# Kernel optimization log

Hardware: AMD Instinct MI355X
Metric: run time of the kernel (lower is better)

The kernel has to match this reference:

```python
import jax, jax.numpy as jnp
import numpy as np

D_MODEL = 1024
N_HEADS = 16
BLOCK = 256
NEG = -1e9


def setup_inputs() -> dict:
    key = jax.random.key(0)
    ks = jax.random.split(key, 5)
    B, S, D = 4, 4096, D_MODEL
    scale = 0.02
    inp = {
        "x": jax.random.normal(ks[0], (B, S, D), dtype=jnp.float32),
        "Wq": jax.random.normal(ks[1], (D, D), dtype=jnp.float32) * scale,
        "bq": jnp.zeros((D,), dtype=jnp.float32),
        "Wk": jax.random.normal(ks[2], (D, D), dtype=jnp.float32) * scale,
        "bk": jnp.zeros((D,), dtype=jnp.float32),
        "Wv": jax.random.normal(ks[3], (D, D), dtype=jnp.float32) * scale,
        "bv": jnp.zeros((D,), dtype=jnp.float32),
        "Wo": jax.random.normal(ks[4], (D, D), dtype=jnp.float32) * scale,
        "bo": jnp.zeros((D,), dtype=jnp.float32),
    }
    return inp


def _local_attention(x, Wq, bq, Wk, bk, Wv, bv, Wo, bo):
    B, S, D = x.shape
    h, dh, bs = N_HEADS, D // N_HEADS, BLOCK
    pad_len = (bs - S % bs) % bs
    if pad_len > 0:
        x = jnp.pad(x, ((0, 0), (0, pad_len), (0, 0)))
    Sp = x.shape[1]
    nb = Sp // bs
    # independent local blocks: [B*nb, bs, D]
    xb = x.reshape(B * nb, bs, D)

    def proj(W, b):
        # [N, bs, D] -> [N, h, bs, dh]
        y = xb @ W + b
        return y.reshape(B * nb, bs, h, dh).transpose(0, 2, 1, 3)

    q = proj(Wq, bq)
    k = proj(Wk, bk)
    v = proj(Wv, bv)

    scores = jnp.einsum('nhqd,nhkd->nhqk', q, k) / jnp.sqrt(jnp.asarray(dh, x.dtype))
    causal = jnp.tril(jnp.ones((bs, bs), dtype=bool))  # block-local causal mask
    scores = jnp.where(causal, scores, jnp.asarray(NEG, x.dtype))
    probs = jax.nn.softmax(scores, axis=-1)
    out = jnp.einsum('nhqk,nhkd->nhqd', probs, v)
    out = out.transpose(0, 2, 1, 3).reshape(B, Sp, D)
    if pad_len > 0:
        out = out[:, :S, :]
    return out @ Wo + bo


def reference(x, Wq, bq, Wk, bk, Wv, bv, Wo, bo):
    return _local_attention(x, Wq, bq, Wk, bk, Wv, bv, Wo, bo)
```

## Files before the change

kernel.cpp:

```cpp
#include <hip/hip_runtime.h>
#include <cstdint>
#include <cstddef>

typedef unsigned short u16;
typedef __attribute__((ext_vector_type(8))) short s16x8;
typedef __attribute__((ext_vector_type(8))) unsigned short u16x8;
typedef __attribute__((ext_vector_type(4))) float f32x4;

#define D_MODEL 1024
#define DH 64
#define BS 256

__device__ __forceinline__ u16 f2bf(float f) {
  union { float f; unsigned int i; } x; x.f = f;
  unsigned int r = x.i + 0x7fffu + ((x.i >> 16) & 1u);
  return (u16)(r >> 16);
}

__device__ __forceinline__ void gl_lds16(const u16* g, u16* l) {
  __builtin_amdgcn_global_load_lds((const __attribute__((address_space(1))) void*)g,
                                   (__attribute__((address_space(3))) void*)l, 16, 0, 0);
}

__device__ __forceinline__ unsigned lds_off(const u16* p) {
  return (unsigned)(uintptr_t)(const __attribute__((address_space(3))) u16*)p;
}

__global__ __launch_bounds__(256) void cast_x(const float* __restrict__ x, u16* __restrict__ xb) {
  int i = (blockIdx.x * 256 + threadIdx.x) * 8;
  f32x4 a0 = *(const f32x4*)(x + i);
  f32x4 a1 = *(const f32x4*)(x + i + 4);
  u16x8 v;
#pragma unroll
  for (int j = 0; j < 4; ++j) { v[j] = f2bf(a0[j]); v[j + 4] = f2bf(a1[j]); }
  *(u16x8*)(xb + i) = v;
}

__global__ __launch_bounds__(256) void transpose_w(const float* __restrict__ w0,
                                                   const float* __restrict__ w1,
                                                   const float* __restrict__ w2,
                                                   const float* __restrict__ w3,
                                                   u16* __restrict__ out) {
  __shared__ u16 tile[64][65];
  const int z = blockIdx.z;
  const float* W = (z == 0) ? w0 : (z == 1) ? w1 : (z == 2) ? w2 : w3;
  u16* O = out + (size_t)z * (D_MODEL * D_MODEL);
  const int kb = blockIdx.y * 64, nb = blockIdx.x * 64;
  const int t = threadIdx.x;
#pragma unroll
  for (int i = 0; i < 16; ++i) {
    int e = i * 256 + t;
    int r = e >> 6, c = e & 63;
    tile[r][c] = f2bf(W[(size_t)(kb + r) * D_MODEL + nb + c]);
  }
  __syncthreads();
#pragma unroll
  for (int i = 0; i < 16; ++i) {
    int e = i * 256 + t;
    int r = e >> 6, c = e & 63;
    O[(size_t)(nb + r) * D_MODEL + kb + c] = tile[c][r];
  }
}


#define TIU 16384
#define HIU 8192

__device__ __forceinline__ void stage_half(const u16* __restrict__ src, int rowG0, int k0,
                                           u16* ldst, int tid) {
#pragma unroll
  for (int i = 0; i < 2; ++i) {
    int c = i * 512 + tid;
    int cs = c ^ (((c >> 5) & 1) << 1);
    gl_lds16(src + (size_t)(rowG0 + (cs >> 3)) * D_MODEL + k0 + (cs & 7) * 8,
             ldst + c * 8);
  }
}

#define NOPX ((void)0)
#define BARX() __builtin_amdgcn_s_barrier()
#define VMW(N) asm volatile("s_waitcnt vmcnt(" #N ")" ::: "memory")
#define SBAR() __builtin_amdgcn_sched_barrier(0)

#define DSR128(dst, b, off) asm volatile("ds_read_b128 %0, %1 offset:" #off : "=v"(dst) : "v"(b))

#define LDA8(P, MH) do { \
  const unsigned _b = ((P) ? aB1 : aB0) + (MH) * 8192u; \
  DSR128(a[0][0], _b, 0);    DSR128(a[0][1], _b, 64); \
  DSR128(a[1][0], _b, 2048); DSR128(a[1][1], _b, 2112); \
  DSR128(a[2][0], _b, 4096); DSR128(a[2][1], _b, 4160); \
  DSR128(a[3][0], _b, 6144); DSR128(a[3][1], _b, 6208); \
} while (0)

#define LDB4(P, NH) do { \
  const unsigned _b = ((P) ? bB1 : bB0) + (NH) * 4096u; \
  DSR128(b[NH][0][0], _b, 0);    DSR128(b[NH][0][1], _b, 64); \
  DSR128(b[NH][1][0], _b, 2048); DSR128(b[NH][1][1], _b, 2112); \
} while (0)

#define MF16(MH, NH) do { \
  __builtin_amdgcn_s_setprio(1); \
  _Pragma("unroll") for (int kk = 0; kk < 2; ++kk) \
  _Pragma("unroll") for (int mt = 0; mt < 4; ++mt) \
  _Pragma("unroll") for (int nt = 0; nt < 2; ++nt) \
    acc[(MH) * 4 + mt][(NH) * 2 + nt] = __builtin_amdgcn_mfma_f32_16x16x32_bf16( \
        a[mt][kk], b[NH][nt][kk], acc[(MH) * 4 + mt][(NH) * 2 + nt], 0, 0, 0); \
  __builtin_amdgcn_s_setprio(0); \
} while (0)

#define STA(T, H) stage_half(A, rowBase + (H) * 128, (T) * 64, As + ((T) & 1) * TIU + (H) * HIU, t)
#define STB(T, H) stage_half(W, colBase + (H) * 128, (T) * 64, Bs + ((T) & 1) * TIU + (H) * HIU, t)

#define PWAIT() do { BARX(); asm volatile("s_waitcnt lgkmcnt(0)"); SBAR(); } while (0)

#define KTILE(P, S1, S2, S3, S4, WAIT) do { \
  LDA8(P, 0); LDB4(P, 0); S1; PWAIT();            MF16(0, 0); BARX(); \
  LDB4(P, 1);             S2; PWAIT();            MF16(0, 1); BARX(); \
  LDA8(P, 1);             S3; PWAIT();            MF16(1, 1); BARX(); \
                    S4; WAIT; BARX(); SBAR();     MF16(1, 0); BARX(); \
} while (0)

template <int MODE, int NCB>
__global__ __launch_bounds__(512, 2) void gemm8(
    const u16* __restrict__ A, const u16* __restrict__ W,
    const float* __restrict__ b0, const float* __restrict__ b1, const float* __restrict__ b2,
    void* __restrict__ o0, void* __restrict__ o1, void* __restrict__ o2) {
  __shared__ u16 As[2 * TIU];
  __shared__ u16 Bs[2 * TIU];

  const int nwg = gridDim.x;
  const int wg = blockIdx.x;
  const int swz = (wg & 7) * (nwg >> 3) + (wg >> 3);
  const int rowBase = (swz / NCB) * 256;
  const int colBase = (swz % NCB) * 256;

  const int t = threadIdx.x;
  const int wave = t >> 6, lane = t & 63, l15 = lane & 15, q4 = lane >> 4;
  const int wm = wave >> 2, wn = wave & 3;
  const int qx = (q4 * 8) ^ ((lane & 4) << 2);
  const int arow = wm * 128 + l15;
  const int brow = wn * 64 + l15;

  const unsigned aB0 = lds_off(As) + (unsigned)arow * 128u + (unsigned)qx * 2u;
  const unsigned aB1 = aB0 + 32768u;
  const unsigned bB0 = lds_off(Bs) + (unsigned)brow * 128u + (unsigned)qx * 2u;
  const unsigned bB1 = bB0 + 32768u;

  f32x4 acc[8][4];
#pragma unroll
  for (int i = 0; i < 8; ++i)
#pragma unroll
    for (int j = 0; j < 4; ++j) acc[i][j] = {0.f, 0.f, 0.f, 0.f};

  s16x8 a[4][2];
  s16x8 b[2][2][2];

  STB(0, 0); STB(0, 1); STA(0, 0); STA(0, 1);
  VMW(4);
  STB(1, 0); STB(1, 1); STA(1, 0);
  VMW(6);
  BARX();

#pragma unroll 1
  for (int tg = 0; tg < 14; tg += 2) {
    KTILE(0, STA(tg + 1, 1), STB(tg + 2, 0), STB(tg + 2, 1), STA(tg + 2, 0), VMW(6));
    KTILE(1, STA(tg + 2, 1), STB(tg + 3, 0), STB(tg + 3, 1), STA(tg + 3, 0), VMW(6));
  }
  KTILE(0, STA(15, 1), NOPX, NOPX, NOPX, VMW(0));
  KTILE(1, NOPX, NOPX, NOPX, NOPX, NOPX);

  if constexpr (MODE == 0) {
    const int z = colBase >> 10;
    const float* bias = (z == 0) ? b0 : (z == 1) ? b1 : b2;
    u16* Out = (u16*)((z == 0) ? o0 : (z == 1) ? o1 : o2);
    const int colL = (colBase & 1023) + wn * 64;
    float bv[4];
#pragma unroll
    for (int ni = 0; ni < 4; ++ni) bv[ni] = bias[colL + ni * 16 + l15];
#pragma unroll
    for (int mi = 0; mi < 8; ++mi) {
#pragma unroll
      for (int r = 0; r < 4; ++r) {
        size_t row = (size_t)(rowBase + wm * 128 + mi * 16 + q4 * 4 + r);
#pragma unroll
        for (int ni = 0; ni < 4; ++ni)
          Out[row * D_MODEL + colL + ni * 16 + l15] = f2bf(acc[mi][ni][r] + bv[ni]);
      }
    }
  } else {
    float* Out = (float*)o0;
    const int colL = colBase + wn * 64;
    float bv[4];
#pragma unroll
    for (int ni = 0; ni < 4; ++ni) bv[ni] = b0[colL + ni * 16 + l15];
#pragma unroll
    for (int mi = 0; mi < 8; ++mi) {
#pragma unroll
      for (int r = 0; r < 4; ++r) {
        size_t row = (size_t)(rowBase + wm * 128 + mi * 16 + q4 * 4 + r);
#pragma unroll
        for (int ni = 0; ni < 4; ++ni)
          Out[row * D_MODEL + colL + ni * 16 + l15] = acc[mi][ni][r] + bv[ni];
      }
    }
  }
}

__global__ __launch_bounds__(128) void attn(const u16* __restrict__ Q, const u16* __restrict__ K,
                                            const u16* __restrict__ V, u16* __restrict__ O) {
  __shared__ u16 vt[64 * 264];
  __shared__ u16 pl[2 * 16 * 264];
  const int g = blockIdx.x;
  const int n = g >> 4, h = g & 15;
  const size_t base = (size_t)n * BS * D_MODEL + (size_t)h * DH;
  const u16* Qb = Q + base;
  const u16* Kb = K + base;
  const u16* Vb = V + base;
  u16* Ob = O + base;
  const int t = threadIdx.x, wave = t >> 6, lane = t & 63, l15 = lane & 15, q4 = lane >> 4;

#pragma unroll
  for (int i = 0; i < 16; ++i) {
    int p = i * 128 + t;
    int d = p & 63, tok8 = p >> 6;
    u16x8 v;
#pragma unroll
    for (int j = 0; j < 8; ++j) v[j] = Vb[(size_t)(tok8 * 8 + j) * D_MODEL + d];
    *(u16x8*)(vt + d * 264 + tok8 * 8) = v;
  }
  __syncthreads();

  u16* pw = pl + wave * 16 * 264;

  for (int pass = 0; pass < 8; ++pass) {
    const int r0 = pass * 32 + wave * 16;
    const int a = r0 >> 4;

    s16x8 aq[2];
#pragma unroll
    for (int kk = 0; kk < 2; ++kk)
      aq[kk] = *(const s16x8*)(Qb + (size_t)(r0 + l15) * D_MODEL + kk * 32 + q4 * 8);

    f32x4 sc[16];
#pragma unroll
    for (int i = 0; i < 16; ++i) sc[i] = {0.f, 0.f, 0.f, 0.f};

#pragma unroll
    for (int nt = 0; nt < 16; ++nt) {
      if (nt <= a) {
#pragma unroll
        for (int kk = 0; kk < 2; ++kk) {
          s16x8 bk = *(const s16x8*)(Kb + (size_t)(nt * 16 + l15) * D_MODEL + kk * 32 + q4 * 8);
          sc[nt] = __builtin_amdgcn_mfma_f32_16x16x32_bf16(aq[kk], bk, sc[nt], 0, 0, 0);
        }
      }
    }

    float mrow[4] = {-3e38f, -3e38f, -3e38f, -3e38f};
#pragma unroll
    for (int nt = 0; nt < 16; ++nt) {
      if (nt <= a) {
#pragma unroll
        for (int r = 0; r < 4; ++r) {
          int col = nt * 16 + l15;
          int row = r0 + q4 * 4 + r;
          float s = (col > row) ? -1.0e9f : sc[nt][r] * 0.125f;
          sc[nt][r] = s;
          mrow[r] = fmaxf(mrow[r], s);
        }
      }
    }
#pragma unroll
    for (int r = 0; r < 4; ++r)
#pragma unroll
      for (int off = 1; off < 16; off <<= 1)
        mrow[r] = fmaxf(mrow[r], __shfl_xor(mrow[r], off, 64));

    float lrow[4] = {0.f, 0.f, 0.f, 0.f};
#pragma unroll
    for (int nt = 0; nt < 16; ++nt) {
      if (nt <= a) {
#pragma unroll
        for (int r = 0; r < 4; ++r) {
          float e = exp2f((sc[nt][r] - mrow[r]) * 1.44269504f);
          sc[nt][r] = e;
          lrow[r] += e;
        }
      }
    }
#pragma unroll
    for (int r = 0; r < 4; ++r)
#pragma unroll
      for (int off = 1; off < 16; off <<= 1)
        lrow[r] += __shfl_xor(lrow[r], off, 64);

#pragma unroll
    for (int nt = 0; nt < 16; ++nt) {
      if (nt <= a) {
#pragma unroll
        for (int r = 0; r < 4; ++r)
          pw[(q4 * 4 + r) * 264 + nt * 16 + l15] = f2bf(sc[nt][r]);
      }
    }
    if ((a & 1) == 0) {
#pragma unroll
      for (int r = 0; r < 4; ++r)
        pw[(q4 * 4 + r) * 264 + (a + 1) * 16 + l15] = 0;
    }
    const int ktmax = (a + 2) >> 1;

    f32x4 oc[4];
#pragma unroll
    for (int i = 0; i < 4; ++i) oc[i] = {0.f, 0.f, 0.f, 0.f};
#pragma unroll
    for (int kt = 0; kt < 8; ++kt) {
      if (kt < ktmax) {
        s16x8 ap = *(const s16x8*)(pw + l15 * 264 + kt * 32 + q4 * 8);
#pragma unroll
        for (int dt = 0; dt < 4; ++dt) {
          s16x8 bv = *(const s16x8*)(vt + (dt * 16 + l15) * 264 + kt * 32 + q4 * 8);
          oc[dt] = __builtin_amdgcn_mfma_f32_16x16x32_bf16(ap, bv, oc[dt], 0, 0, 0);
        }
      }
    }

    float inv[4];
#pragma unroll
    for (int r = 0; r < 4; ++r) inv[r] = 1.0f / lrow[r];

#pragma unroll
    for (int dt = 0; dt < 4; ++dt)
#pragma unroll
      for (int r = 0; r < 4; ++r)
        pw[(q4 * 4 + r) * 264 + dt * 16 + l15] = f2bf(oc[dt][r] * inv[r]);
#pragma unroll
    for (int k = 0; k < 2; ++k) {
      int c2 = k * 64 + lane;
      int row = c2 >> 3, c8 = (c2 & 7) * 8;
      u16x8 v = *(const u16x8*)(pw + row * 264 + c8);
      *(u16x8*)(Ob + (size_t)(r0 + row) * D_MODEL + c8) = v;
    }
  }
}

extern "C" void kernel_launch(void* const* d_in, const int* in_sizes, int n_in,
                              void* d_out, int out_size, void* d_ws, size_t ws_size,
                              hipStream_t stream) {
  const float* x  = (const float*)d_in[0];
  const float* Wq = (const float*)d_in[1];
  const float* bq = (const float*)d_in[2];
  const float* Wk = (const float*)d_in[3];
  const float* bk = (const float*)d_in[4];
  const float* Wv = (const float*)d_in[5];
  const float* bv = (const float*)d_in[6];
  const float* Wo = (const float*)d_in[7];
  const float* bo = (const float*)d_in[8];
  float* out = (float*)d_out;

  u16* ws = (u16*)d_ws;
  u16* Wt = ws;
  u16* Xb = ws + (size_t)4 * 1048576;
  u16* Qw = Xb + (size_t)16777216;
  u16* Kw = Qw + (size_t)16777216;
  u16* Vw = Kw + (size_t)16777216;
  u16* Ow = Qw;

  cast_x<<<dim3(8192), 256, 0, stream>>>(x, Xb);
  transpose_w<<<dim3(16, 16, 4), 256, 0, stream>>>(Wq, Wk, Wv, Wo, Wt);
  gemm8<0, 12><<<dim3(768), 512, 0, stream>>>(Xb, Wt, bq, bk, bv, Qw, Kw, Vw);
  attn<<<dim3(64 * 16), 128, 0, stream>>>(Qw, Kw, Vw, Ow);
  gemm8<1, 4><<<dim3(256), 512, 0, stream>>>(Ow, Wt + (size_t)3 * 1048576, bo,
                                             nullptr, nullptr, out, nullptr, nullptr);
}
```

Baseline: 382.1 us.

## Use full XOR LDS swizzle for GEMM tiles, partial lgkm wait, MFMA priority hints

Replaces the GEMM's LDS swizzle, which flipped one bit based on the row, with a full 3-bit XOR of the 16-byte chunk index by row, applied consistently on the global-to-LDS staging side and the ds_read address side. The aim is to remove LDS bank conflicts on the b128 reads. It also adds an lgkmcnt(8) partial wait before the first barrier of each k-tile and wraps the attention MFMA loops in s_setprio raises. If the staging and read swizzles ever disagree, the GEMM output is wrong.

```diff
diff --git a/kernel.cpp b/kernel.cpp
--- a/kernel.cpp
+++ b/kernel.cpp
@@ -71,7 +71,7 @@
 #pragma unroll
   for (int i = 0; i < 2; ++i) {
     int c = i * 512 + tid;
-    int cs = c ^ (((c >> 5) & 1) << 1);
+    int cs = c ^ ((c >> 3) & 7);
     gl_lds16(src + (size_t)(rowG0 + (cs >> 3)) * D_MODEL + k0 + (cs & 7) * 8,
              ldst + c * 8);
   }
@@ -81,21 +81,22 @@
 #define BARX() __builtin_amdgcn_s_barrier()
 #define VMW(N) asm volatile("s_waitcnt vmcnt(" #N ")" ::: "memory")
 #define SBAR() __builtin_amdgcn_sched_barrier(0)
+#define LGK8() asm volatile("s_waitcnt lgkmcnt(8)")
 
 #define DSR128(dst, b, off) asm volatile("ds_read_b128 %0, %1 offset:" #off : "=v"(dst) : "v"(b))
 
 #define LDA8(P, MH) do { \
-  const unsigned _b = ((P) ? aB1 : aB0) + (MH) * 8192u; \
-  DSR128(a[0][0], _b, 0);    DSR128(a[0][1], _b, 64); \
-  DSR128(a[1][0], _b, 2048); DSR128(a[1][1], _b, 2112); \
-  DSR128(a[2][0], _b, 4096); DSR128(a[2][1], _b, 4160); \
-  DSR128(a[3][0], _b, 6144); DSR128(a[3][1], _b, 6208); \
+  const unsigned _o = (P) * 32768u + (MH) * 8192u; \
+  DSR128(a[0][0], aK0 + _o, 0);    DSR128(a[0][1], aK1 + _o, 0); \
+  DSR128(a[1][0], aK0 + _o, 2048); DSR128(a[1][1], aK1 + _o, 2048); \
+  DSR128(a[2][0], aK0 + _o, 4096); DSR128(a[2][1], aK1 + _o, 4096); \
+  DSR128(a[3][0], aK0 + _o, 6144); DSR128(a[3][1], aK1 + _o, 6144); \
 } while (0)
 
 #define LDB4(P, NH) do { \
-  const unsigned _b = ((P) ? bB1 : bB0) + (NH) * 4096u; \
-  DSR128(b[NH][0][0], _b, 0);    DSR128(b[NH][0][1], _b, 64); \
-  DSR128(b[NH][1][0], _b, 2048); DSR128(b[NH][1][1], _b, 2112); \
+  const unsigned _o = (P) * 32768u + (NH) * 4096u; \
+  DSR128(b[NH][0][0], bK0 + _o, 0);    DSR128(b[NH][0][1], bK1 + _o, 0); \
+  DSR128(b[NH][1][0], bK0 + _o, 2048); DSR128(b[NH][1][1], bK1 + _o, 2048); \
 } while (0)
 
 #define MF16(MH, NH) do { \
@@ -114,10 +115,10 @@
 #define PWAIT() do { BARX(); asm volatile("s_waitcnt lgkmcnt(0)"); SBAR(); } while (0)
 
 #define KTILE(P, S1, S2, S3, S4, WAIT) do { \
-  LDA8(P, 0); LDB4(P, 0); S1; PWAIT();            MF16(0, 0); BARX(); \
-  LDB4(P, 1);             S2; PWAIT();            MF16(0, 1); BARX(); \
-  LDA8(P, 1);             S3; PWAIT();            MF16(1, 1); BARX(); \
-                    S4; WAIT; BARX(); SBAR();     MF16(1, 0); BARX(); \
+  LDA8(P, 0); LDB4(P, 0); S1; LGK8(); PWAIT();  MF16(0, 0); BARX(); \
+  LDB4(P, 1);             S2; PWAIT();          MF16(0, 1); BARX(); \
+  LDA8(P, 1);             S3; PWAIT();          MF16(1, 1); BARX(); \
+                    S4; WAIT; BARX(); SBAR();   MF16(1, 0); BARX(); \
 } while (0)
 
 template <int MODE, int NCB>
@@ -137,14 +138,14 @@
   const int t = threadIdx.x;
   const int wave = t >> 6, lane = t & 63, l15 = lane & 15, q4 = lane >> 4;
   const int wm = wave >> 2, wn = wave & 3;
-  const int qx = (q4 * 8) ^ ((lane & 4) << 2);
   const int arow = wm * 128 + l15;
   const int brow = wn * 64 + l15;
 
-  const unsigned aB0 = lds_off(As) + (unsigned)arow * 128u + (unsigned)qx * 2u;
-  const unsigned aB1 = aB0 + 32768u;
-  const unsigned bB0 = lds_off(Bs) + (unsigned)brow * 128u + (unsigned)qx * 2u;
-  const unsigned bB1 = bB0 + 32768u;
+  const unsigned swzc = (unsigned)((q4 ^ (l15 & 7)) << 4);
+  const unsigned aK0 = lds_off(As) + (unsigned)arow * 128u + swzc;
+  const unsigned aK1 = aK0 ^ 64u;
+  const unsigned bK0 = lds_off(Bs) + (unsigned)brow * 128u + swzc;
+  const unsigned bK1 = bK0 ^ 64u;
 
   f32x4 acc[8][4];
 #pragma unroll
@@ -245,6 +246,7 @@
 #pragma unroll
     for (int i = 0; i < 16; ++i) sc[i] = {0.f, 0.f, 0.f, 0.f};
 
+    __builtin_amdgcn_s_setprio(1);
 #pragma unroll
     for (int nt = 0; nt < 16; ++nt) {
       if (nt <= a) {
@@ -255,6 +257,7 @@
         }
       }
     }
+    __builtin_amdgcn_s_setprio(0);
 
     float mrow[4] = {-3e38f, -3e38f, -3e38f, -3e38f};
 #pragma unroll
@@ -312,6 +315,7 @@
     f32x4 oc[4];
 #pragma unroll
     for (int i = 0; i < 4; ++i) oc[i] = {0.f, 0.f, 0.f, 0.f};
+    __builtin_amdgcn_s_setprio(1);
 #pragma unroll
     for (int kt = 0; kt < 8; ++kt) {
       if (kt < ktmax) {
@@ -323,6 +327,7 @@
         }
       }
     }
+    __builtin_amdgcn_s_setprio(0);
 
     float inv[4];
 #pragma unroll
```

After: 371.0 us. -2.9%, faster.
